# Optimization experiments

Hardware: AMD Instinct MI355X
Metric: run time of the kernel (lower is better)

## Reference

```python
import jax, jax.numpy as jnp
import numpy as np

B = 2
C = 256
NH = 8
DH = C // NH
NL = 4
NP = 4
NLAYERS = 6
DFF = 1024
SHAPES = [(128, 128), (64, 64), (32, 32), (16, 16)]
LQ = sum(h * w for h, w in SHAPES)
STARTS = np.cumsum([0] + [h * w for h, w in SHAPES])[:-1].tolist()


def _ln(x, g, b, eps=1e-5):
    mu = jnp.mean(x, -1, keepdims=True)
    var = jnp.mean((x - mu) ** 2, -1, keepdims=True)
    return (x - mu) * jax.lax.rsqrt(var + eps) * g + b


def _ref_points():
    # centers of each cell, normalized to [0,1]; valid_ratios == 1 (masks=None path)
    pts = []
    for (h, w) in SHAPES:
        ry = (np.arange(h) + 0.5) / h
        rx = (np.arange(w) + 0.5) / w
        gy, gx = np.meshgrid(ry, rx, indexing='ij')
        pts.append(np.stack([gx.reshape(-1), gy.reshape(-1)], -1))
    return jnp.asarray(np.concatenate(pts, 0), jnp.float32)  # [LQ,2] (x,y)


def _bilinear(vf, loc, Hl, Wl):
    # vf: [B,NH,S,DH] flattened level features; loc: [B,LQ,NH,NP,2] in [0,1]
    # grid_sample semantics: bilinear, zero padding, align_corners=False
    x = loc[..., 0] * Wl - 0.5
    y = loc[..., 1] * Hl - 0.5
    x0 = jnp.floor(x)
    y0 = jnp.floor(y)
    wx = x - x0
    wy = y - y0
    out = 0.0
    for dx, dy, w in ((0, 0, (1 - wx) * (1 - wy)), (1, 0, wx * (1 - wy)),
                      (0, 1, (1 - wx) * wy), (1, 1, wx * wy)):
        xi = x0 + dx
        yi = y0 + dy
        valid = (xi >= 0) & (xi < Wl) & (yi >= 0) & (yi < Hl)
        idx = (jnp.clip(yi, 0, Hl - 1) * Wl + jnp.clip(xi, 0, Wl - 1)).astype(jnp.int32)
        idx = jnp.transpose(idx, (0, 2, 1, 3)).reshape(B, NH, -1)  # [B,NH,LQ*NP]
        g = jnp.take_along_axis(vf, idx[..., None], axis=2)        # [B,NH,LQ*NP,DH]
        wgt = jnp.transpose(w * valid, (0, 2, 1, 3)).reshape(B, NH, -1)
        out = out + g * wgt[..., None]
    return out.reshape(B, NH, LQ, NP, DH)


def _forward(src0, src1, src2, src3, pos0, pos1, pos2, pos3, level_embed,
             Woff, boff, Wattn, battn, Wval, bval, Wout, bout,
             g1, b1, Wff1, bff1, Wff2, bff2, g2, b2):
    srcs = [src0, src1, src2, src3]
    poss = [pos0, pos1, pos2, pos3]
    src = jnp.concatenate([s.reshape(B, C, -1).transpose(0, 2, 1) for s in srcs], 1)
    pos = jnp.concatenate([p.reshape(B, C, -1).transpose(0, 2, 1) + level_embed[l][None, None]
                           for l, p in enumerate(poss)], 1)
    ref = _ref_points()  # [LQ,2]
    norm_wh = jnp.asarray([[w, h] for (h, w) in SHAPES], jnp.float32)  # offset_normalizer
    x = src
    for l in range(NLAYERS):
        q = x + pos
        off = (q @ Woff[l] + boff[l]).reshape(B, LQ, NH, NL, NP, 2)
        attn = jax.nn.softmax((q @ Wattn[l] + battn[l]).reshape(B, LQ, NH, NL * NP), -1)
        attn = attn.reshape(B, LQ, NH, NL, NP)
        val = (x @ Wval[l] + bval[l]).reshape(B, LQ, NH, DH)
        loc = ref[None, :, None, None, None, :] + off / norm_wh[None, None, None, :, None, :]
        out = jnp.zeros((B, NH, LQ, DH), x.dtype)
        for lv, (h, w) in enumerate(SHAPES):
            s0 = STARTS[lv]
            vf = val[:, s0:s0 + h * w].transpose(0, 2, 1, 3)   # [B,NH,S,DH]
            samp = _bilinear(vf, loc[:, :, :, lv], h, w)       # [B,NH,LQ,NP,DH]
            a = attn[:, :, :, lv].transpose(0, 2, 1, 3)        # [B,NH,LQ,NP]
            out = out + jnp.einsum('bhqpd,bhqp->bhqd', samp, a)
        out = out.transpose(0, 2, 1, 3).reshape(B, LQ, C) @ Wout[l] + bout[l]
        x = _ln(x + out, g1[l], b1[l])
        ff = jax.nn.relu(x @ Wff1[l] + bff1[l]) @ Wff2[l] + bff2[l]
        x = _ln(x + ff, g2[l], b2[l])
    return x


def setup_inputs() -> dict:
    key = jax.random.key(0)
    ks = jax.random.split(key, 20)
    d = {}
    for i, (h, w) in enumerate(SHAPES):
        d[f'src{i}'] = jax.random.normal(ks[i], (B, C, h, w), jnp.float32)
        d[f'pos{i}'] = jax.random.normal(ks[4 + i], (B, C, h, w), jnp.float32) * 0.1
    d['level_embed'] = jax.random.normal(ks[8], (NL, C), jnp.float32)

    def lin(k, fi, fo, scale=None):
        s = scale if scale is not None else 1.0 / np.sqrt(fi)
        return jax.random.normal(k, (NLAYERS, fi, fo), jnp.float32) * s

    d['Woff'] = lin(ks[9], C, NH * NL * NP * 2, 0.01)
    d['boff'] = jax.random.uniform(ks[10], (NLAYERS, NH * NL * NP * 2), jnp.float32, -0.5, 0.5)
    d['Wattn'] = lin(ks[11], C, NH * NL * NP)
    d['battn'] = jnp.zeros((NLAYERS, NH * NL * NP), jnp.float32)
    d['Wval'] = lin(ks[12], C, C)
    d['bval'] = jnp.zeros((NLAYERS, C), jnp.float32)
    d['Wout'] = lin(ks[13], C, C)
    d['bout'] = jnp.zeros((NLAYERS, C), jnp.float32)
    d['g1'] = jnp.ones((NLAYERS, C), jnp.float32)
    d['b1'] = jnp.zeros((NLAYERS, C), jnp.float32)
    d['Wff1'] = lin(ks[14], C, DFF)
    d['bff1'] = jnp.zeros((NLAYERS, DFF), jnp.float32)
    d['Wff2'] = lin(ks[15], DFF, C)
    d['bff2'] = jnp.zeros((NLAYERS, C), jnp.float32)
    d['g2'] = jnp.ones((NLAYERS, C), jnp.float32)
    d['b2'] = jnp.zeros((NLAYERS, C), jnp.float32)
    return d


def reference(src0, src1, src2, src3, pos0, pos1, pos2, pos3, level_embed,
              Woff, boff, Wattn, battn, Wval, bval, Wout, bout,
              g1, b1, Wff1, bff1, Wff2, bff2, g2, b2):
    return _forward(src0, src1, src2, src3, pos0, pos1, pos2, pos3, level_embed,
                    Woff, boff, Wattn, battn, Wval, bval, Wout, bout,
                    g1, b1, Wff1, bff1, Wff2, bff2, g2, b2)
```

## Files before the change

kernel.cpp:

```cpp
#include <hip/hip_runtime.h>
#include <hip/hip_bf16.h>
#include <hip/hip_fp16.h>
#include <math.h>

namespace {
constexpr int B_   = 2;
constexpr int C_   = 256;
constexpr int NH_  = 8;
constexpr int DH_  = 32;
constexpr int NP_  = 4;
constexpr int DFF_ = 1024;
constexpr int LQ_  = 21760;
constexpr int M_   = B_ * LQ_;
}

typedef __bf16  bf16x8 __attribute__((ext_vector_type(8)));
typedef short   s16x8  __attribute__((ext_vector_type(8)));
typedef float   f32x4  __attribute__((ext_vector_type(4)));

#define AS1 __attribute__((address_space(1)))
#define AS3 __attribute__((address_space(3)))

static __device__ __forceinline__ unsigned short f2bf(float f) {
    return __builtin_bit_cast(unsigned short, __float2bfloat16(f));
}
static __device__ __forceinline__ float bf2f(unsigned short u) {
    return __bfloat162float(__builtin_bit_cast(__hip_bfloat16, u));
}

__global__ void k_wt(const float* __restrict__ in, __hip_bfloat16* __restrict__ out,
                     int K, int N, int outStride)
{
    __shared__ float tile[32][33];
    int n0 = blockIdx.x * 32, k0 = blockIdx.y * 32;
    const float* inl = in + (size_t)blockIdx.z * K * N;
    __hip_bfloat16* outl = out + (size_t)blockIdx.z * outStride;
    for (int i = threadIdx.y; i < 32; i += 8)
        tile[i][threadIdx.x] = inl[(size_t)(k0 + i) * N + n0 + threadIdx.x];
    __syncthreads();
    for (int i = threadIdx.y; i < 32; i += 8)
        outl[(size_t)(n0 + i) * K + k0 + threadIdx.x] = __float2bfloat16(tile[threadIdx.x][i]);
}

__global__ __launch_bounds__(256) void k_assemble2(
    const float* __restrict__ s0, const float* __restrict__ s1,
    const float* __restrict__ s2, const float* __restrict__ s3,
    const float* __restrict__ p0, const float* __restrict__ p1,
    const float* __restrict__ p2, const float* __restrict__ p3,
    const float* __restrict__ lev, float* __restrict__ x,
    __hip_bfloat16* __restrict__ xbf, __hip_bfloat16* __restrict__ posbf,
    __hip_bfloat16* __restrict__ qbf)
{
    int bid = blockIdx.x;
    int lv, rem, HW, S0;
    const float *sp, *pp;
    if (bid < 8192)       { lv = 0; rem = bid;         HW = 16384; S0 = 0;     sp = s0; pp = p0; }
    else if (bid < 10240) { lv = 1; rem = bid - 8192;  HW = 4096;  S0 = 16384; sp = s1; pp = p1; }
    else if (bid < 10752) { lv = 2; rem = bid - 10240; HW = 1024;  S0 = 20480; sp = s2; pp = p2; }
    else                  { lv = 3; rem = bid - 10752; HW = 256;   S0 = 21504; sp = s3; pp = p3; }
    int sptiles = HW >> 5;
    int spt = rem % sptiles;
    int ct  = (rem / sptiles) & 7;
    int b   = rem / (sptiles * 8);
    int sp0 = spt * 32, c0 = ct * 32;

    __shared__ float ts[32][33], tp[32][33];
    int tx = threadIdx.x & 31, ty = threadIdx.x >> 5;
#pragma unroll
    for (int i = 0; i < 4; i++) {
        int c = c0 + ty + i * 8;
        size_t si = ((size_t)(b * C_ + c)) * HW + sp0 + tx;
        ts[ty + i * 8][tx] = sp[si];
        tp[ty + i * 8][tx] = pp[si];
    }
    __syncthreads();
#pragma unroll
    for (int i = 0; i < 4; i++) {
        int s = S0 + sp0 + ty + i * 8;
        int c = c0 + tx;
        float sv = ts[tx][ty + i * 8];
        float pv = tp[tx][ty + i * 8] + lev[lv * C_ + c];
        size_t idx = ((size_t)(b * LQ_ + s)) * C_ + c;
        x[idx]     = sv;
        xbf[idx]   = __float2bfloat16(sv);
        posbf[idx] = __float2bfloat16(pv);
        qbf[idx]   = __float2bfloat16(sv + pv);
    }
}

__global__ __launch_bounds__(256) void k_gemm_qa(
    const __hip_bfloat16* __restrict__ A,
    const __hip_bfloat16* __restrict__ Wq,
    const float* __restrict__ boff, const float* __restrict__ battn,
    __half* __restrict__ offh, float* __restrict__ attb, int M)
{
    constexpr int K = 256;
    __shared__ char As[128 * 128];
    __shared__ char Bs[128 * 128];
    int t = threadIdx.x, w = t >> 6, lane = t & 63;
    int m0 = blockIdx.x * 128, n0 = blockIdx.y * 128;
    int wm = w >> 1, wn = w & 1;

    f32x4 acc[4][4] = {};
    int rowoff  = lane >> 3;
    int colswz  = ((lane & 7) ^ (lane >> 3)) << 3;

    for (int kt = 0; kt < K; kt += 64) {
#pragma unroll
        for (int j = 0; j < 4; j++) {
            int rowbase = w * 32 + j * 8;
            const __hip_bfloat16* srcA = A  + (size_t)(m0 + rowbase + rowoff) * K + kt + colswz;
            const __hip_bfloat16* srcB = Wq + (size_t)(n0 + rowbase + rowoff) * K + kt + colswz;
            __builtin_amdgcn_global_load_lds(
                (const AS1 void*)srcA, (AS3 void*)(As + rowbase * 128), 16, 0, 0);
            __builtin_amdgcn_global_load_lds(
                (const AS1 void*)srcB, (AS3 void*)(Bs + rowbase * 128), 16, 0, 0);
        }
        __syncthreads();
#pragma unroll
        for (int k0 = 0; k0 < 64; k0 += 32) {
            int kb = k0 * 2 + (lane >> 4) * 16;
            bf16x8 af[4], bfr[4];
#pragma unroll
            for (int mi = 0; mi < 4; mi++) {
                int r = wm * 64 + mi * 16 + (lane & 15);
                s16x8 raw = *(const s16x8*)(As + r * 128 + (kb ^ ((r & 7) << 4)));
                af[mi] = __builtin_bit_cast(bf16x8, raw);
            }
#pragma unroll
            for (int ni = 0; ni < 4; ni++) {
                int r = wn * 64 + ni * 16 + (lane & 15);
                s16x8 raw = *(const s16x8*)(Bs + r * 128 + (kb ^ ((r & 7) << 4)));
                bfr[ni] = __builtin_bit_cast(bf16x8, raw);
            }
#pragma unroll
            for (int mi = 0; mi < 4; mi++)
#pragma unroll
                for (int ni = 0; ni < 4; ni++)
                    acc[mi][ni] = __builtin_amdgcn_mfma_f32_16x16x32_bf16(
                        af[mi], bfr[ni], acc[mi][ni], 0, 0, 0);
        }
        __syncthreads();
    }

    if (blockIdx.y == 2) {
#pragma unroll
        for (int ni = 0; ni < 4; ni++) {
            int col = wn * 64 + ni * 16 + (lane & 15);
            float bb = battn[col];
#pragma unroll
            for (int mi = 0; mi < 4; mi++) {
                int row = m0 + wm * 64 + mi * 16 + ((lane >> 4) << 2);
#pragma unroll
                for (int r = 0; r < 4; r++)
                    attb[(size_t)(row + r) * 128 + col] = acc[mi][ni][r] + bb;
            }
        }
    } else {
#pragma unroll
        for (int ni = 0; ni < 4; ni++) {
            int col = n0 + wn * 64 + ni * 16 + (lane & 15);
            float bb = boff[col];
#pragma unroll
            for (int mi = 0; mi < 4; mi++) {
                int row = m0 + wm * 64 + mi * 16 + ((lane >> 4) << 2);
#pragma unroll
                for (int r = 0; r < 4; r++)
                    offh[(size_t)(row + r) * 256 + col] = __float2half(acc[mi][ni][r] + bb);
            }
        }
    }
}

static __device__ __forceinline__ void stage_x64(
    const __hip_bfloat16* __restrict__ src, int m0, char* xs, int w, int lane)
{
    int r  = lane >> 5;
    int gl = lane & 31;
#pragma unroll
    for (int j = 0; j < 8; j++) {
        int row = (j * 4 + w) * 2 + r;
        int gsw = gl ^ (row & 7);
        const __hip_bfloat16* s = src + (size_t)(m0 + row) * 256 + gsw * 8;
        __builtin_amdgcn_global_load_lds(
            (const AS1 void*)s, (AS3 void*)(xs + (j * 4 + w) * 1024), 16, 0, 0);
    }
}

template<bool WRITE_Q>
static __device__ __forceinline__ void ln_epilogue64(
    f32x4 (&acc)[4][4], int m0, int w, int lane,
    const float* bias, float* xio, __hip_bfloat16* xbf,
    const float* g, const float* beta,
    const __hip_bfloat16* posb, __hip_bfloat16* qout,
    float (*sred1)[4], float (*sred2)[4])
{
    int cl = lane & 15;
    int rg = (lane >> 4) << 2;
    float bcol[4], gcol[4], btcol[4];
#pragma unroll
    for (int ni = 0; ni < 4; ni++) {
        int col = w * 64 + ni * 16 + cl;
        bcol[ni]  = bias[col];
        gcol[ni]  = g[col];
        btcol[ni] = beta[col];
    }

#pragma unroll
    for (int mi = 0; mi < 4; mi++)
#pragma unroll
    for (int r = 0; r < 4; r++) {
        int lr  = mi * 16 + rg + r;
        int row = m0 + lr;
        float s = 0.f;
#pragma unroll
        for (int ni = 0; ni < 4; ni++) {
            int col = w * 64 + ni * 16 + cl;
            float v = acc[mi][ni][r] + bcol[ni] + xio[(size_t)row * 256 + col];
            acc[mi][ni][r] = v;
            s += v;
        }
        s += __shfl_xor(s, 1); s += __shfl_xor(s, 2);
        s += __shfl_xor(s, 4); s += __shfl_xor(s, 8);
        if (cl == 0) sred1[lr][w] = s;
    }
    __syncthreads();

    float mu[4][4];
#pragma unroll
    for (int mi = 0; mi < 4; mi++)
#pragma unroll
    for (int r = 0; r < 4; r++) {
        int lr = mi * 16 + rg + r;
        mu[mi][r] = (sred1[lr][0] + sred1[lr][1] + sred1[lr][2] + sred1[lr][3]) * (1.f / 256.f);
        float s2 = 0.f;
#pragma unroll
        for (int ni = 0; ni < 4; ni++) {
            float d = acc[mi][ni][r] - mu[mi][r];
            s2 += d * d;
        }
        s2 += __shfl_xor(s2, 1); s2 += __shfl_xor(s2, 2);
        s2 += __shfl_xor(s2, 4); s2 += __shfl_xor(s2, 8);
        if (cl == 0) sred2[lr][w] = s2;
    }
    __syncthreads();

#pragma unroll
    for (int mi = 0; mi < 4; mi++)
#pragma unroll
    for (int r = 0; r < 4; r++) {
        int lr  = mi * 16 + rg + r;
        int row = m0 + lr;
        float var = (sred2[lr][0] + sred2[lr][1] + sred2[lr][2] + sred2[lr][3]) * (1.f / 256.f);
        float rstd = rsqrtf(var + 1e-5f);
#pragma unroll
        for (int ni = 0; ni < 4; ni++) {
            int col = w * 64 + ni * 16 + cl;
            size_t idx = (size_t)row * 256 + col;
            float o = (acc[mi][ni][r] - mu[mi][r]) * rstd * gcol[ni] + btcol[ni];
            xio[idx] = o;
            xbf[idx] = __float2bfloat16(o);
            if (WRITE_Q)
                qout[idx] = __float2bfloat16(o + bf2f(__builtin_bit_cast(unsigned short, posb[idx])));
        }
    }
}

template<bool RELU>
__global__ __launch_bounds__(256) void k_gemm_direct(
    const __hip_bfloat16* __restrict__ A,
    const __hip_bfloat16* __restrict__ Wt,
    const float* __restrict__ bias,
    __hip_bfloat16* __restrict__ out, int N)
{
    __shared__ char xs[64 * 512];
    int t = threadIdx.x, w = t >> 6, lane = t & 63;
    int m0 = blockIdx.x * 64, n0 = blockIdx.y * 256;

    stage_x64(A, m0, xs, w, lane);
    asm volatile("s_waitcnt vmcnt(0)" ::: "memory");
    __builtin_amdgcn_s_barrier();

    f32x4 acc[4][4] = {};
#pragma unroll
    for (int k0 = 0; k0 < 256; k0 += 32) {
        int kb = k0 * 2 + (lane >> 4) * 16;
        bf16x8 af[4], bw[4];
#pragma unroll
        for (int mi = 0; mi < 4; mi++) {
            int r = mi * 16 + (lane & 15);
            s16x8 raw = *(const s16x8*)(xs + r * 512 + (kb ^ ((r & 7) << 4)));
            af[mi] = __builtin_bit_cast(bf16x8, raw);
        }
#pragma unroll
        for (int ni = 0; ni < 4; ni++) {
            int col = n0 + w * 64 + ni * 16 + (lane & 15);
            bw[ni] = *(const bf16x8*)(Wt + (size_t)col * 256 + k0 + (lane >> 4) * 8);
        }
#pragma unroll
        for (int mi = 0; mi < 4; mi++)
#pragma unroll
            for (int ni = 0; ni < 4; ni++)
                acc[mi][ni] = __builtin_amdgcn_mfma_f32_16x16x32_bf16(
                    af[mi], bw[ni], acc[mi][ni], 0, 0, 0);
    }

#pragma unroll
    for (int ni = 0; ni < 4; ni++) {
        int col = n0 + w * 64 + ni * 16 + (lane & 15);
        float bb = bias[col];
#pragma unroll
        for (int mi = 0; mi < 4; mi++) {
            int row = m0 + mi * 16 + ((lane >> 4) << 2);
#pragma unroll
            for (int r = 0; r < 4; r++) {
                float v = acc[mi][ni][r] + bb;
                if (RELU) v = fmaxf(v, 0.f);
                out[(size_t)(row + r) * N + col] = __float2bfloat16(v);
            }
        }
    }
}

template<bool WRITE_Q>
__global__ __launch_bounds__(256) void k_out(
    const __hip_bfloat16* __restrict__ A,
    const __hip_bfloat16* __restrict__ Wt,
    const float* __restrict__ bias,
    float* __restrict__ xio, __hip_bfloat16* __restrict__ xbf,
    const float* __restrict__ g, const float* __restrict__ beta,
    const __hip_bfloat16* __restrict__ posb, __hip_bfloat16* __restrict__ qout)
{
    __shared__ char xs[64 * 512];
    __shared__ float sred1[64][4];
    __shared__ float sred2[64][4];

    int t = threadIdx.x, w = t >> 6, lane = t & 63;
    int m0 = blockIdx.x * 64;

    stage_x64(A, m0, xs, w, lane);
    asm volatile("s_waitcnt vmcnt(0)" ::: "memory");
    __builtin_amdgcn_s_barrier();

    f32x4 acc[4][4] = {};
#pragma unroll
    for (int k0 = 0; k0 < 256; k0 += 32) {
        int kb = k0 * 2 + (lane >> 4) * 16;
        bf16x8 af[4], bw[4];
#pragma unroll
        for (int mi = 0; mi < 4; mi++) {
            int r = mi * 16 + (lane & 15);
            s16x8 raw = *(const s16x8*)(xs + r * 512 + (kb ^ ((r & 7) << 4)));
            af[mi] = __builtin_bit_cast(bf16x8, raw);
        }
#pragma unroll
        for (int ni = 0; ni < 4; ni++) {
            int col = w * 64 + ni * 16 + (lane & 15);
            bw[ni] = *(const bf16x8*)(Wt + (size_t)col * 256 + k0 + (lane >> 4) * 8);
        }
#pragma unroll
        for (int mi = 0; mi < 4; mi++)
#pragma unroll
            for (int ni = 0; ni < 4; ni++)
                acc[mi][ni] = __builtin_amdgcn_mfma_f32_16x16x32_bf16(
                    af[mi], bw[ni], acc[mi][ni], 0, 0, 0);
    }
    __syncthreads();

    ln_epilogue64<WRITE_Q>(acc, m0, w, lane, bias, xio, xbf, g, beta, posb, qout,
                           sred1, sred2);
}

template<bool WRITE_Q>
__global__ __launch_bounds__(512) void k_ff2ln(
    const __hip_bfloat16* __restrict__ A,
    const __hip_bfloat16* __restrict__ Wt,
    const float* __restrict__ bias,
    float* __restrict__ xio, __hip_bfloat16* __restrict__ xbf,
    const float* __restrict__ g, const float* __restrict__ beta,
    const __hip_bfloat16* __restrict__ posb, __hip_bfloat16* __restrict__ qout,
    int M, int K)
{
    __shared__ char As[2][128 * 128];
    __shared__ float sred1[128][4];
    __shared__ float sred2[128][4];

    int t = threadIdx.x, w = t >> 6, lane = t & 63;
    int m0 = blockIdx.x * 128;
    int wm = w >> 2, wn = w & 3;

    f32x4 acc[4][4] = {};

    int rowoff  = lane >> 3;
    int colswz  = ((lane & 7) ^ rowoff) << 3;

    auto STAGE_A = [&](char* Ab, int kt) {
#pragma unroll
        for (int j = 0; j < 2; j++) {
            int rowbase = w * 16 + j * 8;
            const __hip_bfloat16* srcA = A + (size_t)(m0 + rowbase + rowoff) * K + kt + colswz;
            __builtin_amdgcn_global_load_lds(
                (const AS1 void*)srcA, (AS3 void*)(Ab + rowbase * 128), 16, 0, 0);
        }
    };

    STAGE_A(As[0], 0);
    asm volatile("s_waitcnt vmcnt(0)" ::: "memory");
    __builtin_amdgcn_s_barrier();

    const int nt = K >> 6;
    int cur = 0;
    for (int tt = 0; tt < nt; ++tt) {
        if (tt + 1 < nt) STAGE_A(As[cur ^ 1], (tt + 1) << 6);
        const char* Ab = As[cur];
        int ktb = tt << 6;
#pragma unroll
        for (int k0 = 0; k0 < 64; k0 += 32) {
            int kb = k0 * 2 + (lane >> 4) * 16;
            bf16x8 af[4], bw[4];
#pragma unroll
            for (int mi = 0; mi < 4; mi++) {
                int r = wm * 64 + mi * 16 + (lane & 15);
                s16x8 raw = *(const s16x8*)(Ab + r * 128 + (kb ^ ((r & 7) << 4)));
                af[mi] = __builtin_bit_cast(bf16x8, raw);
            }
#pragma unroll
            for (int ni = 0; ni < 4; ni++) {
                int col = wn * 64 + ni * 16 + (lane & 15);
                bw[ni] = *(const bf16x8*)(Wt + (size_t)col * K + ktb + k0 + (lane >> 4) * 8);
            }
#pragma unroll
            for (int mi = 0; mi < 4; mi++)
#pragma unroll
                for (int ni = 0; ni < 4; ni++)
                    acc[mi][ni] = __builtin_amdgcn_mfma_f32_16x16x32_bf16(
                        af[mi], bw[ni], acc[mi][ni], 0, 0, 0);
        }
        asm volatile("s_waitcnt vmcnt(0)" ::: "memory");
        __builtin_amdgcn_s_barrier();
        cur ^= 1;
    }

    int cl = lane & 15;
    int rg = (lane >> 4) << 2;
    float bcol[4], gcol[4], btcol[4];
#pragma unroll
    for (int ni = 0; ni < 4; ni++) {
        int col = wn * 64 + ni * 16 + cl;
        bcol[ni]  = bias[col];
        gcol[ni]  = g[col];
        btcol[ni] = beta[col];
    }

#pragma unroll
    for (int mi = 0; mi < 4; mi++)
#pragma unroll
    for (int r = 0; r < 4; r++) {
        int lr  = wm * 64 + mi * 16 + rg + r;
        int row = m0 + lr;
        float s = 0.f;
#pragma unroll
        for (int ni = 0; ni < 4; ni++) {
            int col = wn * 64 + ni * 16 + cl;
            float v = acc[mi][ni][r] + bcol[ni] + xio[(size_t)row * 256 + col];
            acc[mi][ni][r] = v;
            s += v;
        }
        s += __shfl_xor(s, 1); s += __shfl_xor(s, 2);
        s += __shfl_xor(s, 4); s += __shfl_xor(s, 8);
        if (cl == 0) sred1[lr][wn] = s;
    }
    __syncthreads();

    float mu[4][4];
#pragma unroll
    for (int mi = 0; mi < 4; mi++)
#pragma unroll
    for (int r = 0; r < 4; r++) {
        int lr = wm * 64 + mi * 16 + rg + r;
        mu[mi][r] = (sred1[lr][0] + sred1[lr][1] + sred1[lr][2] + sred1[lr][3]) * (1.f / 256.f);
        float s2 = 0.f;
#pragma unroll
        for (int ni = 0; ni < 4; ni++) {
            float d = acc[mi][ni][r] - mu[mi][r];
            s2 += d * d;
        }
        s2 += __shfl_xor(s2, 1); s2 += __shfl_xor(s2, 2);
        s2 += __shfl_xor(s2, 4); s2 += __shfl_xor(s2, 8);
        if (cl == 0) sred2[lr][wn] = s2;
    }
    __syncthreads();

#pragma unroll
    for (int mi = 0; mi < 4; mi++)
#pragma unroll
    for (int r = 0; r < 4; r++) {
        int lr  = wm * 64 + mi * 16 + rg + r;
        int row = m0 + lr;
        float var = (sred2[lr][0] + sred2[lr][1] + sred2[lr][2] + sred2[lr][3]) * (1.f / 256.f);
        float rstd = rsqrtf(var + 1e-5f);
#pragma unroll
        for (int ni = 0; ni < 4; ni++) {
            int col = wn * 64 + ni * 16 + cl;
            size_t idx = (size_t)row * 256 + col;
            float o = (acc[mi][ni][r] - mu[mi][r]) * rstd * gcol[ni] + btcol[ni];
            xio[idx] = o;
            xbf[idx] = __float2bfloat16(o);
            if (WRITE_Q)
                qout[idx] = __float2bfloat16(o + bf2f(__builtin_bit_cast(unsigned short, posb[idx])));
        }
    }
}

__global__ __launch_bounds__(256) void k_sample4(const __hip_bfloat16* __restrict__ val,
                                                 const __half* __restrict__ offh,
                                                 const float* __restrict__ logits,
                                                 __hip_bfloat16* __restrict__ out)
{
    __shared__ int2 sIW[4 * 64 * 17];

    int t  = threadIdx.x;
    int qb = blockIdx.x;

#pragma unroll
    for (int it = 0; it < 4; it++) {
        int item = t + it * 256;
        int qi = item >> 7;
        int pt = item & 127;
        int bs = qb * 8 + qi;
        int b  = bs / LQ_;
        int s  = bs % LQ_;
        int h  = pt >> 4, lv = (pt >> 2) & 3;

        float lg = logits[(size_t)bs * 128 + pt];
        float mx = lg;
#pragma unroll
        for (int m = 1; m < 16; m <<= 1) mx = fmaxf(mx, __shfl_xor(mx, m));
        float ex = __expf(lg - mx);
        float sm = ex;
#pragma unroll
        for (int m = 1; m < 16; m <<= 1) sm += __shfl_xor(sm, m);
        float aw = ex / sm;

        int p0, Wq;
        if (s < 16384)      { p0 = s;         Wq = 128; }
        else if (s < 20480) { p0 = s - 16384; Wq = 64;  }
        else if (s < 21504) { p0 = s - 20480; Wq = 32;  }
        else                { p0 = s - 21504; Wq = 16;  }
        float invWq = 1.f / (float)Wq;
        float refx = ((p0 % Wq) + 0.5f) * invWq;
        float refy = ((p0 / Wq) + 0.5f) * invWq;

        int W  = 128 >> lv;
        int S0 = (65536 - (65536 >> (2 * lv))) / 3;
        float fW = (float)W;

        __half2 o2 = ((const __half2*)(offh + (size_t)bs * 256))[pt];
        float ox = __low2float(o2), oy = __high2float(o2);
        float xx = refx * fW + ox - 0.5f;
        float yy = refy * fW + oy - 0.5f;
        float x0f = floorf(xx), y0f = floorf(yy);
        float wx = xx - x0f, wy = yy - y0f;
        int x0 = (int)x0f, y0 = (int)y0f;
        int x1 = x0 + 1, y1 = y0 + 1;
        bool vx0 = (x0 >= 0) & (x0 < W), vx1 = (x1 >= 0) & (x1 < W);
        bool vy0 = (y0 >= 0) & (y0 < W), vy1 = (y1 >= 0) & (y1 < W);
        int cx0 = min(max(x0, 0), W - 1), cx1 = min(max(x1, 0), W - 1);
        int cy0 = min(max(y0, 0), W - 1), cy1 = min(max(y1, 0), W - 1);

        int rowbase = (b * LQ_ + S0) * C_ + h * DH_;
        int g  = item >> 4;
        int pj = pt & 15;
        int i00 = (rowbase + (cy0 * W + cx0) * C_) * 2;
        int i10 = (rowbase + (cy0 * W + cx1) * C_) * 2;
        int i01 = (rowbase + (cy1 * W + cx0) * C_) * 2;
        int i11 = (rowbase + (cy1 * W + cx1) * C_) * 2;
        float w00 = aw * (1.f - wx) * (1.f - wy) * ((vx0 & vy0) ? 1.f : 0.f);
        float w10 = aw * wx * (1.f - wy) * ((vx1 & vy0) ? 1.f : 0.f);
        float w01 = aw * (1.f - wx) * wy * ((vx0 & vy1) ? 1.f : 0.f);
        float w11 = aw * wx * wy * ((vx1 & vy1) ? 1.f : 0.f);
        sIW[(0 * 64 + g) * 17 + pj] = make_int2(i00, __float_as_int(w00));
        sIW[(1 * 64 + g) * 17 + pj] = make_int2(i10, __float_as_int(w10));
        sIW[(2 * 64 + g) * 17 + pj] = make_int2(i01, __float_as_int(w01));
        sIW[(3 * 64 + g) * 17 + pj] = make_int2(i11, __float_as_int(w11));
    }
    __syncthreads();

    {
        int g  = t >> 2;
        int dq = t & 3;
        int bs = qb * 8 + (g >> 3);
        int h  = g & 7;
        int dbyte = dq * 16;

        const char* vbase = (const char*)val;
        float a0 = 0.f, a1 = 0.f, a2 = 0.f, a3 = 0.f;
        float a4 = 0.f, a5 = 0.f, a6 = 0.f, a7 = 0.f;
#pragma unroll
        for (int j = 0; j < 16; j++) {
#pragma unroll
            for (int k = 0; k < 4; k++) {
                int2 iw = sIW[(k * 64 + g) * 17 + j];
                float w = __int_as_float(iw.y);
                uint4 u = *(const uint4*)(vbase + iw.x + dbyte);
                a0 = fmaf(w, __builtin_bit_cast(float, u.x << 16), a0);
                a1 = fmaf(w, __builtin_bit_cast(float, u.x & 0xffff0000u), a1);
                a2 = fmaf(w, __builtin_bit_cast(float, u.y << 16), a2);
                a3 = fmaf(w, __builtin_bit_cast(float, u.y & 0xffff0000u), a3);
                a4 = fmaf(w, __builtin_bit_cast(float, u.z << 16), a4);
                a5 = fmaf(w, __builtin_bit_cast(float, u.z & 0xffff0000u), a5);
                a6 = fmaf(w, __builtin_bit_cast(float, u.w << 16), a6);
                a7 = fmaf(w, __builtin_bit_cast(float, u.w & 0xffff0000u), a7);
            }
        }
        uint4 o;
        o.x = (unsigned)f2bf(a0) | ((unsigned)f2bf(a1) << 16);
        o.y = (unsigned)f2bf(a2) | ((unsigned)f2bf(a3) << 16);
        o.z = (unsigned)f2bf(a4) | ((unsigned)f2bf(a5) << 16);
        o.w = (unsigned)f2bf(a6) | ((unsigned)f2bf(a7) << 16);
        *(uint4*)((char*)out + (size_t)bs * 512 + h * 64 + dbyte) = o;
    }
}

extern "C" void kernel_launch(void* const* d_in, const int* in_sizes, int n_in,
                              void* d_out, int out_size, void* d_ws, size_t ws_size,
                              hipStream_t stream)
{
    const float* src_[4] = {(const float*)d_in[0], (const float*)d_in[2],
                            (const float*)d_in[4], (const float*)d_in[6]};
    const float* pos_[4] = {(const float*)d_in[1], (const float*)d_in[3],
                            (const float*)d_in[5], (const float*)d_in[7]};
    const float* lev   = (const float*)d_in[8];
    const float* Woff  = (const float*)d_in[9];
    const float* boff  = (const float*)d_in[10];
    const float* Wattn = (const float*)d_in[11];
    const float* battn = (const float*)d_in[12];
    const float* Wval  = (const float*)d_in[13];
    const float* bval  = (const float*)d_in[14];
    const float* Wout  = (const float*)d_in[15];
    const float* bout  = (const float*)d_in[16];
    const float* g1    = (const float*)d_in[17];
    const float* b1    = (const float*)d_in[18];
    const float* Wff1  = (const float*)d_in[19];
    const float* bff1  = (const float*)d_in[20];
    const float* Wff2  = (const float*)d_in[21];
    const float* bff2  = (const float*)d_in[22];
    const float* g2    = (const float*)d_in[23];
    const float* b2    = (const float*)d_in[24];

    float* x = (float*)d_out;
    size_t MC = (size_t)M_ * C_;

    __hip_bfloat16* pos_bf = (__hip_bfloat16*)d_ws;
    __hip_bfloat16* q_bf   = pos_bf + MC;
    __hip_bfloat16* x_bf   = q_bf + MC;
    __half* offh           = (__half*)(x_bf + MC);
    float*  attb           = (float*)(offh + MC);
    __hip_bfloat16* val_bf = (__hip_bfloat16*)(attb + (size_t)M_ * 128);
    __hip_bfloat16* pad_bf = val_bf + MC;
    __hip_bfloat16* ffh_bf = (__hip_bfloat16*)offh;
    __hip_bfloat16* wbf    = pad_bf + MC;

    __hip_bfloat16* wq    = wbf;
    __hip_bfloat16* wvalt = wq    + 6 * 98304;
    __hip_bfloat16* woutt = wvalt + 6 * 65536;
    __hip_bfloat16* wff1t = woutt + 6 * 65536;
    __hip_bfloat16* wff2t = wff1t + 6 * 262144;

    dim3 blk(256);
    dim3 tblk(32, 8);

    k_wt<<<dim3(8, 8, 6),  tblk, 0, stream>>>(Woff,  wq,               256, 256,  98304);
    k_wt<<<dim3(4, 8, 6),  tblk, 0, stream>>>(Wattn, wq + 256 * 256,   256, 128,  98304);
    k_wt<<<dim3(8, 8, 6),  tblk, 0, stream>>>(Wval,  wvalt,            256, 256,  65536);
    k_wt<<<dim3(8, 8, 6),  tblk, 0, stream>>>(Wout,  woutt,            256, 256,  65536);
    k_wt<<<dim3(32, 8, 6), tblk, 0, stream>>>(Wff1,  wff1t,            256, 1024, 262144);
    k_wt<<<dim3(8, 32, 6), tblk, 0, stream>>>(Wff2,  wff2t,            1024, 256, 262144);

    k_assemble2<<<10880, blk, 0, stream>>>(
        src_[0], src_[1], src_[2], src_[3],
        pos_[0], pos_[1], pos_[2], pos_[3], lev, x, x_bf, pos_bf, q_bf);

    for (int l = 0; l < 6; l++) {
        k_gemm_qa<<<dim3(M_ / 128, 3), blk, 0, stream>>>(
            q_bf, wq + (size_t)l * 98304, boff + l * 256, battn + l * 128,
            offh, attb, M_);

        k_gemm_direct<false><<<dim3(M_ / 64, 1), blk, 0, stream>>>(
            x_bf, wvalt + (size_t)l * 65536, bval + l * 256, val_bf, 256);

        k_sample4<<<M_ / 8, blk, 0, stream>>>(val_bf, offh, attb, q_bf);

        k_out<false><<<M_ / 64, blk, 0, stream>>>(
            q_bf, woutt + (size_t)l * 65536, bout + l * 256,
            x, x_bf, g1 + l * 256, b1 + l * 256, nullptr, nullptr);

        k_gemm_direct<true><<<dim3(M_ / 64, 4), blk, 0, stream>>>(
            x_bf, wff1t + (size_t)l * 262144, bff1 + l * DFF_, ffh_bf, DFF_);

        if (l < 5)
            k_ff2ln<true><<<M_ / 128, 512, 0, stream>>>(
                ffh_bf, wff2t + (size_t)l * 262144, bff2 + l * C_,
                x, x_bf, g2 + l * 256, b2 + l * 256, pos_bf, q_bf, M_, DFF_);
        else
            k_ff2ln<false><<<M_ / 128, 512, 0, stream>>>(
                ffh_bf, wff2t + (size_t)l * 262144, bff2 + l * C_,
                x, x_bf, g2 + l * 256, b2 + l * 256, nullptr, nullptr, M_, DFF_);
    }
}
```

Measured before the change: 2.188 ms.

## Stage weight tiles through LDS for FF1 and FF2 GEMMs

Replaces the FF1 direct-load GEMM (64-row tiles) with a new 128x128 MFMA kernel that stages both A and weight tiles through swizzled LDS. The FF2+LayerNorm kernel now double-buffers its 256-column weight tile in LDS alongside A, instead of reading weight fragments straight from global memory. The aim is to cut repeated global and L2 traffic for the weights and raise reuse per block. In exchange, LDS use grows to about 96KB per block in FF2, which can lower occupancy, and the new FF1 kernel is single-buffered with a barrier on every K step.

Result: faster. 1.881 ms (-14.0%).

```diff
diff --git a/kernel.cpp b/kernel.cpp
--- a/kernel.cpp
+++ b/kernel.cpp
@@ -88,6 +88,83 @@
     }
 }
 
+template<bool RELU, bool BF16OUT>
+__global__ __launch_bounds__(256) void k_gemm_mfma(
+    const __hip_bfloat16* __restrict__ A,
+    const __hip_bfloat16* __restrict__ Wt,
+    const float* __restrict__ bias,
+    void* __restrict__ Co,
+    int M, int N, int K)
+{
+    __shared__ char As[128 * 128];
+    __shared__ char Bs[128 * 128];
+    int t = threadIdx.x, w = t >> 6, lane = t & 63;
+    int m0 = blockIdx.x * 128, n0 = blockIdx.y * 128;
+    int wm = w >> 1, wn = w & 1;
+
+    f32x4 acc[4][4] = {};
+
+    int rowoff  = lane >> 3;
+    int colswz  = ((lane & 7) ^ (lane >> 3)) << 3;
+
+    for (int kt = 0; kt < K; kt += 64) {
+#pragma unroll
+        for (int j = 0; j < 4; j++) {
+            int rowbase = w * 32 + j * 8;
+            const __hip_bfloat16* srcA = A  + (size_t)(m0 + rowbase + rowoff) * K + kt + colswz;
+            const __hip_bfloat16* srcB = Wt + (size_t)(n0 + rowbase + rowoff) * K + kt + colswz;
+            __builtin_amdgcn_global_load_lds(
+                (const AS1 void*)srcA, (AS3 void*)(As + rowbase * 128), 16, 0, 0);
+            __builtin_amdgcn_global_load_lds(
+                (const AS1 void*)srcB, (AS3 void*)(Bs + rowbase * 128), 16, 0, 0);
+        }
+        __syncthreads();
+#pragma unroll
+        for (int k0 = 0; k0 < 64; k0 += 32) {
+            int kb = k0 * 2 + (lane >> 4) * 16;
+            bf16x8 af[4], bfr[4];
+#pragma unroll
+            for (int mi = 0; mi < 4; mi++) {
+                int r = wm * 64 + mi * 16 + (lane & 15);
+                s16x8 raw = *(const s16x8*)(As + r * 128 + (kb ^ ((r & 7) << 4)));
+                af[mi] = __builtin_bit_cast(bf16x8, raw);
+            }
+#pragma unroll
+            for (int ni = 0; ni < 4; ni++) {
+                int r = wn * 64 + ni * 16 + (lane & 15);
+                s16x8 raw = *(const s16x8*)(Bs + r * 128 + (kb ^ ((r & 7) << 4)));
+                bfr[ni] = __builtin_bit_cast(bf16x8, raw);
+            }
+#pragma unroll
+            for (int mi = 0; mi < 4; mi++)
+#pragma unroll
+                for (int ni = 0; ni < 4; ni++)
+                    acc[mi][ni] = __builtin_amdgcn_mfma_f32_16x16x32_bf16(
+                        af[mi], bfr[ni], acc[mi][ni], 0, 0, 0);
+        }
+        __syncthreads();
+    }
+
+#pragma unroll
+    for (int ni = 0; ni < 4; ni++) {
+        int col = n0 + wn * 64 + ni * 16 + (lane & 15);
+        float bb = bias[col];
+#pragma unroll
+        for (int mi = 0; mi < 4; mi++) {
+            int row = m0 + wm * 64 + mi * 16 + ((lane >> 4) << 2);
+#pragma unroll
+            for (int r = 0; r < 4; r++) {
+                float v = acc[mi][ni][r] + bb;
+                if (RELU) v = fmaxf(v, 0.f);
+                if (BF16OUT)
+                    ((__hip_bfloat16*)Co)[(size_t)(row + r) * N + col] = __float2bfloat16(v);
+                else
+                    ((float*)Co)[(size_t)(row + r) * N + col] = v;
+            }
+        }
+    }
+}
+
 __global__ __launch_bounds__(256) void k_gemm_qa(
     const __hip_bfloat16* __restrict__ A,
     const __hip_bfloat16* __restrict__ Wq,
@@ -372,16 +449,19 @@
 }
 
 template<bool WRITE_Q>
-__global__ __launch_bounds__(512) void k_ff2ln(
+__global__ __launch_bounds__(512) void k_gemm_ln(
     const __hip_bfloat16* __restrict__ A,
     const __hip_bfloat16* __restrict__ Wt,
     const float* __restrict__ bias,
-    float* __restrict__ xio, __hip_bfloat16* __restrict__ xbf,
+    float* __restrict__ xio,
+    __hip_bfloat16* __restrict__ xbf,
     const float* __restrict__ g, const float* __restrict__ beta,
-    const __hip_bfloat16* __restrict__ posb, __hip_bfloat16* __restrict__ qout,
+    const __hip_bfloat16* __restrict__ posb,
+    __hip_bfloat16* __restrict__ qout,
     int M, int K)
 {
     __shared__ char As[2][128 * 128];
+    __shared__ char Bs[2][256 * 128];
     __shared__ float sred1[128][4];
     __shared__ float sred2[128][4];
 
@@ -394,7 +474,7 @@
     int rowoff  = lane >> 3;
     int colswz  = ((lane & 7) ^ rowoff) << 3;
 
-    auto STAGE_A = [&](char* Ab, int kt) {
+    auto STAGE = [&](char* Ab, char* Bb, int kt) {
 #pragma unroll
         for (int j = 0; j < 2; j++) {
             int rowbase = w * 16 + j * 8;
@@ -402,22 +482,29 @@
             __builtin_amdgcn_global_load_lds(
                 (const AS1 void*)srcA, (AS3 void*)(Ab + rowbase * 128), 16, 0, 0);
         }
+#pragma unroll
+        for (int j = 0; j < 4; j++) {
+            int rowbase = w * 32 + j * 8;
+            const __hip_bfloat16* srcB = Wt + (size_t)(rowbase + rowoff) * K + kt + colswz;
+            __builtin_amdgcn_global_load_lds(
+                (const AS1 void*)srcB, (AS3 void*)(Bb + rowbase * 128), 16, 0, 0);
+        }
     };
 
-    STAGE_A(As[0], 0);
+    STAGE(As[0], Bs[0], 0);
     asm volatile("s_waitcnt vmcnt(0)" ::: "memory");
     __builtin_amdgcn_s_barrier();
 
     const int nt = K >> 6;
     int cur = 0;
     for (int tt = 0; tt < nt; ++tt) {
-        if (tt + 1 < nt) STAGE_A(As[cur ^ 1], (tt + 1) << 6);
+        if (tt + 1 < nt) STAGE(As[cur ^ 1], Bs[cur ^ 1], (tt + 1) << 6);
         const char* Ab = As[cur];
-        int ktb = tt << 6;
+        const char* Bb = Bs[cur];
 #pragma unroll
         for (int k0 = 0; k0 < 64; k0 += 32) {
             int kb = k0 * 2 + (lane >> 4) * 16;
-            bf16x8 af[4], bw[4];
+            bf16x8 af[4], bfr[4];
 #pragma unroll
             for (int mi = 0; mi < 4; mi++) {
                 int r = wm * 64 + mi * 16 + (lane & 15);
@@ -426,15 +513,16 @@
             }
 #pragma unroll
             for (int ni = 0; ni < 4; ni++) {
-                int col = wn * 64 + ni * 16 + (lane & 15);
-                bw[ni] = *(const bf16x8*)(Wt + (size_t)col * K + ktb + k0 + (lane >> 4) * 8);
+                int r = wn * 64 + ni * 16 + (lane & 15);
+                s16x8 raw = *(const s16x8*)(Bb + r * 128 + (kb ^ ((r & 7) << 4)));
+                bfr[ni] = __builtin_bit_cast(bf16x8, raw);
             }
 #pragma unroll
             for (int mi = 0; mi < 4; mi++)
 #pragma unroll
                 for (int ni = 0; ni < 4; ni++)
                     acc[mi][ni] = __builtin_amdgcn_mfma_f32_16x16x32_bf16(
-                        af[mi], bw[ni], acc[mi][ni], 0, 0, 0);
+                        af[mi], bfr[ni], acc[mi][ni], 0, 0, 0);
         }
         asm volatile("s_waitcnt vmcnt(0)" ::: "memory");
         __builtin_amdgcn_s_barrier();
@@ -695,15 +783,15 @@
             q_bf, woutt + (size_t)l * 65536, bout + l * 256,
             x, x_bf, g1 + l * 256, b1 + l * 256, nullptr, nullptr);
 
-        k_gemm_direct<true><<<dim3(M_ / 64, 4), blk, 0, stream>>>(
-            x_bf, wff1t + (size_t)l * 262144, bff1 + l * DFF_, ffh_bf, DFF_);
+        k_gemm_mfma<true, true><<<dim3(M_ / 128, 8), blk, 0, stream>>>(
+            x_bf, wff1t + (size_t)l * 262144, bff1 + l * DFF_, ffh_bf, M_, DFF_, C_);
 
         if (l < 5)
-            k_ff2ln<true><<<M_ / 128, 512, 0, stream>>>(
+            k_gemm_ln<true><<<M_ / 128, 512, 0, stream>>>(
                 ffh_bf, wff2t + (size_t)l * 262144, bff2 + l * C_,
                 x, x_bf, g2 + l * 256, b2 + l * 256, pos_bf, q_bf, M_, DFF_);
         else
-            k_ff2ln<false><<<M_ / 128, 512, 0, stream>>>(
+            k_gemm_ln<false><<<M_ / 128, 512, 0, stream>>>(
                 ffh_bf, wff2t + (size_t)l * 262144, bff2 + l * C_,
                 x, x_bf, g2 + l * 256, b2 + l * 256, nullptr, nullptr, M_, DFF_);
     }
```
